# Performance work log

Hardware: AMD Instinct MI355X
Metric: run time of the kernel (lower is better)

Reference implementation:

```python
import jax, jax.numpy as jnp
import numpy as np

N, D, T = 4096, 512, 4096
TEMPERATURE = 0.07
MARGIN = 0.5
CONT_WEIGHT = 1.0
TRIP_WEIGHT = 0.3
EPS = 1e-8        # eps in the log / denominator (matches torch code)
PD_EPS = 1e-6     # F.pairwise_distance default eps added to the difference


def setup_inputs() -> dict:
    key = jax.random.key(0)
    k1, k2, k3 = jax.random.split(key, 3)
    embeddings = jax.random.normal(k1, (N, D), dtype=jnp.float32)
    labels = jax.random.randint(k2, (N,), 0, 256)            # ~16 positives per place
    triplets = jax.random.randint(k3, (T, 3), 0, N)          # (anchor, pos, neg) indices
    return {"embeddings": embeddings, "labels": labels, "triplets": triplets}


def reference(embeddings, labels, triplets):
    # ---- MultiPositiveContrastiveLoss ----
    # F.cosine_similarity normalizes each row with eps=1e-8 on the norm.
    norms = jnp.linalg.norm(embeddings, axis=1, keepdims=True)
    n_emb = embeddings / jnp.maximum(norms, EPS)
    sim = (n_emb @ n_emb.T) / TEMPERATURE                    # [N, N]

    pos_mask = (labels[:, None] == labels[None, :]).astype(embeddings.dtype)
    pos_mask = pos_mask * (1.0 - jnp.eye(sim.shape[0], dtype=embeddings.dtype))

    exp_sim = jnp.exp(sim)
    pos_sum = (exp_sim * pos_mask).sum(axis=1)
    total_sum = exp_sim.sum(axis=1)
    loss = -jnp.log(pos_sum / (total_sum + EPS) + EPS)

    valid = pos_mask.sum(axis=1) > 0
    cnt = valid.sum()
    cont_loss = jnp.where(
        cnt > 0,
        jnp.where(valid, loss, 0.0).sum() / jnp.maximum(cnt, 1).astype(loss.dtype),
        jnp.zeros((), loss.dtype),
    )

    # ---- TripletLoss, vectorized over all triplets (replaces Python loop) ----
    a = embeddings[triplets[:, 0]]   # [T, D]
    p = embeddings[triplets[:, 1]]
    ng = embeddings[triplets[:, 2]]
    pos_dist = jnp.linalg.norm(a - p + PD_EPS, axis=1)
    neg_dist = jnp.linalg.norm(a - ng + PD_EPS, axis=1)
    trip_loss = jnp.maximum(pos_dist - neg_dist + MARGIN, 0.0).mean()

    total = CONT_WEIGHT * cont_loss + TRIP_WEIGHT * trip_loss
    return (total, cont_loss, trip_loss)
```

## Files before the change

kernel.cpp:

```cpp
#include <hip/hip_runtime.h>

#define NN 4096
#define DD 512
#define TT 4096

typedef __bf16 bf16x8 __attribute__((ext_vector_type(8)));
typedef float f32x4 __attribute__((ext_vector_type(4)));

constexpr float INV_TEMP = 1.0f / 0.07f;

__global__ __launch_bounds__(256) void k_normalize(const float* __restrict__ emb,
                                                   __bf16* __restrict__ nemb) {
    int wave = threadIdx.x >> 6, lane = threadIdx.x & 63;
    int row = blockIdx.x * 4 + wave;
    const float4* src = (const float4*)(emb + (size_t)row * DD);
    float4 x0 = src[lane * 2 + 0];
    float4 x1 = src[lane * 2 + 1];
    float ss = x0.x * x0.x + x0.y * x0.y + x0.z * x0.z + x0.w * x0.w +
               x1.x * x1.x + x1.y * x1.y + x1.z * x1.z + x1.w * x1.w;
    #pragma unroll
    for (int m = 1; m < 64; m <<= 1) ss += __shfl_xor(ss, m, 64);
    float inv = 1.0f / fmaxf(sqrtf(ss), 1e-8f);
    bf16x8 v;
    v[0] = (__bf16)(x0.x * inv); v[1] = (__bf16)(x0.y * inv);
    v[2] = (__bf16)(x0.z * inv); v[3] = (__bf16)(x0.w * inv);
    v[4] = (__bf16)(x1.x * inv); v[5] = (__bf16)(x1.y * inv);
    v[6] = (__bf16)(x1.z * inv); v[7] = (__bf16)(x1.w * inv);
    *(bf16x8*)(nemb + (size_t)row * DD + lane * 8) = v;
}

__global__ __launch_bounds__(256) void k_contrast(const __bf16* __restrict__ nemb,
                                                  const int* __restrict__ labels,
                                                  float* __restrict__ posP,
                                                  float* __restrict__ totP,
                                                  float* __restrict__ cntP) {
    __shared__ __attribute__((aligned(16))) __bf16 aSm[128 * 32];
    __shared__ __attribute__((aligned(16))) __bf16 bSm[128 * 32];
    __shared__ int rlab[128];
    __shared__ int clab[128];

    int tid = threadIdx.x;
    int lane = tid & 63, wave = tid >> 6;
    int wr = wave >> 1, wc = wave & 1;
    int l15 = lane & 15, quad = lane >> 4;
    int rowblk = blockIdx.y, colblk = blockIdx.x;
    int row0 = rowblk * 128, col0 = colblk * 128;

    if (tid < 128) rlab[tid] = labels[row0 + tid];
    else           clab[tid - 128] = labels[col0 + tid - 128];

    f32x4 acc[4][4];
    #pragma unroll
    for (int r = 0; r < 4; ++r)
        #pragma unroll
        for (int c = 0; c < 4; ++c) {
            f32x4 z = {0.0f, 0.0f, 0.0f, 0.0f};
            acc[r][c] = z;
        }

    int rA = tid >> 2, sA = tid & 3;

    for (int kt = 0; kt < 16; ++kt) {
        int kb = kt * 32;
        uint4 a0 = *(const uint4*)(nemb + (size_t)(row0 + rA) * DD + kb + sA * 8);
        uint4 a1 = *(const uint4*)(nemb + (size_t)(row0 + rA + 64) * DD + kb + sA * 8);
        uint4 b0 = *(const uint4*)(nemb + (size_t)(col0 + rA) * DD + kb + sA * 8);
        uint4 b1 = *(const uint4*)(nemb + (size_t)(col0 + rA + 64) * DD + kb + sA * 8);
        __syncthreads();
        ((uint4*)aSm)[tid] = a0;
        ((uint4*)aSm)[tid + 256] = a1;
        ((uint4*)bSm)[tid] = b0;
        ((uint4*)bSm)[tid + 256] = b1;
        __syncthreads();

        bf16x8 af[4], bfr[4];
        #pragma unroll
        for (int r = 0; r < 4; ++r)
            af[r] = *(const bf16x8*)(aSm + (wr * 64 + r * 16 + l15) * 32 + quad * 8);
        #pragma unroll
        for (int c = 0; c < 4; ++c)
            bfr[c] = *(const bf16x8*)(bSm + (wc * 64 + c * 16 + l15) * 32 + quad * 8);
        #pragma unroll
        for (int r = 0; r < 4; ++r)
            #pragma unroll
            for (int c = 0; c < 4; ++c)
                acc[r][c] = __builtin_amdgcn_mfma_f32_16x16x32_bf16(af[r], bfr[c], acc[r][c], 0, 0, 0);
    }

    int cl[4];
    #pragma unroll
    for (int c = 0; c < 4; ++c) cl[c] = clab[wc * 64 + c * 16 + l15];

    #pragma unroll
    for (int r = 0; r < 4; ++r) {
        float tv[4] = {0, 0, 0, 0}, pv[4] = {0, 0, 0, 0}, cv[4] = {0, 0, 0, 0};
        int gibase = row0 + wr * 64 + r * 16 + quad * 4;
        int rl[4];
        #pragma unroll
        for (int v = 0; v < 4; ++v) rl[v] = rlab[wr * 64 + r * 16 + quad * 4 + v];
        #pragma unroll
        for (int c = 0; c < 4; ++c) {
            int gj = col0 + wc * 64 + c * 16 + l15;
            #pragma unroll
            for (int v = 0; v < 4; ++v) {
                float e = __expf(acc[r][c][v] * INV_TEMP);
                tv[v] += e;
                bool match = (rl[v] == cl[c]) && ((gibase + v) != gj);
                pv[v] += match ? e : 0.0f;
                cv[v] += match ? 1.0f : 0.0f;
            }
        }
        #pragma unroll
        for (int m = 1; m < 16; m <<= 1) {
            #pragma unroll
            for (int v = 0; v < 4; ++v) {
                tv[v] += __shfl_xor(tv[v], m, 64);
                pv[v] += __shfl_xor(pv[v], m, 64);
                cv[v] += __shfl_xor(cv[v], m, 64);
            }
        }
        if (l15 == 0) {
            #pragma unroll
            for (int v = 0; v < 4; ++v) {
                int gr = gibase + v;
                int idx = gr * 64 + colblk * 2 + wc;
                posP[idx] = pv[v];
                totP[idx] = tv[v];
                cntP[idx] = cv[v];
            }
        }
    }
}

__global__ __launch_bounds__(256) void k_triplet(const float* __restrict__ emb,
                                                 const int* __restrict__ trip,
                                                 float* __restrict__ tl) {
    int wave = threadIdx.x >> 6, lane = threadIdx.x & 63;
    int t = blockIdx.x * 4 + wave;
    int ia = trip[t * 3 + 0], ip = trip[t * 3 + 1], ig = trip[t * 3 + 2];
    const float4* pa = (const float4*)(emb + (size_t)ia * DD);
    const float4* pp = (const float4*)(emb + (size_t)ip * DD);
    const float4* pn = (const float4*)(emb + (size_t)ig * DD);
    float d1 = 0.0f, d2 = 0.0f;
    #pragma unroll
    for (int j = 0; j < 2; ++j) {
        float4 a = pa[lane * 2 + j];
        float4 p = pp[lane * 2 + j];
        float4 n = pn[lane * 2 + j];
        float dx;
        dx = a.x - p.x + 1e-6f; d1 += dx * dx;
        dx = a.y - p.y + 1e-6f; d1 += dx * dx;
        dx = a.z - p.z + 1e-6f; d1 += dx * dx;
        dx = a.w - p.w + 1e-6f; d1 += dx * dx;
        dx = a.x - n.x + 1e-6f; d2 += dx * dx;
        dx = a.y - n.y + 1e-6f; d2 += dx * dx;
        dx = a.z - n.z + 1e-6f; d2 += dx * dx;
        dx = a.w - n.w + 1e-6f; d2 += dx * dx;
    }
    #pragma unroll
    for (int m = 1; m < 64; m <<= 1) {
        d1 += __shfl_xor(d1, m, 64);
        d2 += __shfl_xor(d2, m, 64);
    }
    if (lane == 0) tl[t] = fmaxf(sqrtf(d1) - sqrtf(d2) + 0.5f, 0.0f);
}

__global__ __launch_bounds__(256) void k_rowloss(const float* __restrict__ posP,
                                                 const float* __restrict__ totP,
                                                 const float* __restrict__ cntP,
                                                 float* __restrict__ rloss,
                                                 float* __restrict__ rvalid) {
    int row = blockIdx.x * 256 + threadIdx.x;
    float p = 0.0f, t = 0.0f, c = 0.0f;
    for (int i = 0; i < 64; ++i) {
        p += posP[row * 64 + i];
        t += totP[row * 64 + i];
        c += cntP[row * 64 + i];
    }
    float loss = -logf(p / (t + 1e-8f) + 1e-8f);
    bool valid = c > 0.0f;
    rloss[row] = valid ? loss : 0.0f;
    rvalid[row] = valid ? 1.0f : 0.0f;
}

__global__ __launch_bounds__(256) void k_final(const float* __restrict__ rloss,
                                               const float* __restrict__ rvalid,
                                               const float* __restrict__ tl,
                                               float* __restrict__ out) {
    int tid = threadIdx.x;
    float sl = 0.0f, sv = 0.0f, st = 0.0f;
    for (int i = tid; i < NN; i += 256) {
        sl += rloss[i];
        sv += rvalid[i];
        st += tl[i];
    }
    #pragma unroll
    for (int m = 1; m < 64; m <<= 1) {
        sl += __shfl_xor(sl, m, 64);
        sv += __shfl_xor(sv, m, 64);
        st += __shfl_xor(st, m, 64);
    }
    __shared__ float red[3][4];
    int lane = tid & 63, wave = tid >> 6;
    if (lane == 0) { red[0][wave] = sl; red[1][wave] = sv; red[2][wave] = st; }
    __syncthreads();
    if (tid == 0) {
        float SL = red[0][0] + red[0][1] + red[0][2] + red[0][3];
        float SV = red[1][0] + red[1][1] + red[1][2] + red[1][3];
        float ST = red[2][0] + red[2][1] + red[2][2] + red[2][3];
        float cont = (SV > 0.0f) ? (SL / SV) : 0.0f;
        float trip = ST * (1.0f / (float)TT);
        out[0] = cont + 0.3f * trip;
        out[1] = cont;
        out[2] = trip;
    }
}

extern "C" void kernel_launch(void* const* d_in, const int* in_sizes, int n_in,
                              void* d_out, int out_size, void* d_ws, size_t ws_size,
                              hipStream_t stream) {
    const float* emb = (const float*)d_in[0];
    const int* labels = (const int*)d_in[1];
    const int* trips = (const int*)d_in[2];
    float* out = (float*)d_out;
    char* ws = (char*)d_ws;

    __bf16* nemb  = (__bf16*)(ws);
    float* posP   = (float*)(ws + 4194304);
    float* totP   = (float*)(ws + 5242880);
    float* cntP   = (float*)(ws + 6291456);
    float* rloss  = (float*)(ws + 7340032);
    float* rvalid = (float*)(ws + 7356416);
    float* tl     = (float*)(ws + 7372800);

    k_normalize<<<NN / 4, 256, 0, stream>>>(emb, nemb);
    k_contrast<<<dim3(32, 32), 256, 0, stream>>>(nemb, labels, posP, totP, cntP);
    k_triplet<<<TT / 4, 256, 0, stream>>>(emb, trips, tl);
    k_rowloss<<<NN / 256, 256, 0, stream>>>(posP, totP, cntP, rloss, rvalid);
    k_final<<<1, 256, 0, stream>>>(rloss, rvalid, tl, out);
}
```

Before: 117.4 us.

## Exploit similarity-matrix symmetry by computing only upper-triangular tiles

The contrastive kernel now launches 528 blocks over the upper-triangular 128x128 tiles of the similarity matrix instead of all 1024. Each block decodes its tile coordinates from a triangular index. Off-diagonal tiles also reduce their exp values along columns and write those partial sums into the transposed tile's slots, so about half of the GEMM and exp work is skipped. This costs extra column reductions, extra partial-sum writes, and some integer/sqrt index math per block.

```diff
diff --git a/kernel.cpp b/kernel.cpp
--- a/kernel.cpp
+++ b/kernel.cpp
@@ -43,8 +43,15 @@
     int lane = tid & 63, wave = tid >> 6;
     int wr = wave >> 1, wc = wave & 1;
     int l15 = lane & 15, quad = lane >> 4;
-    int rowblk = blockIdx.y, colblk = blockIdx.x;
+
+    int idx = blockIdx.x;
+    int cb = (int)((sqrtf(8.0f * (float)idx + 1.0f) - 1.0f) * 0.5f);
+    while ((cb + 1) * (cb + 2) / 2 <= idx) ++cb;
+    while (cb * (cb + 1) / 2 > idx) --cb;
+    int rb = idx - cb * (cb + 1) / 2;
+    int rowblk = rb, colblk = cb;
     int row0 = rowblk * 128, col0 = colblk * 128;
+    bool offd = (rowblk != colblk);
 
     if (tid < 128) rlab[tid] = labels[row0 + tid];
     else           clab[tid - 128] = labels[col0 + tid - 128];
@@ -91,6 +98,8 @@
     #pragma unroll
     for (int c = 0; c < 4; ++c) cl[c] = clab[wc * 64 + c * 16 + l15];
 
+    float tT[4] = {0, 0, 0, 0}, pT[4] = {0, 0, 0, 0}, cT[4] = {0, 0, 0, 0};
+
     #pragma unroll
     for (int r = 0; r < 4; ++r) {
         float tv[4] = {0, 0, 0, 0}, pv[4] = {0, 0, 0, 0}, cv[4] = {0, 0, 0, 0};
@@ -104,10 +113,11 @@
             #pragma unroll
             for (int v = 0; v < 4; ++v) {
                 float e = __expf(acc[r][c][v] * INV_TEMP);
-                tv[v] += e;
                 bool match = (rl[v] == cl[c]) && ((gibase + v) != gj);
-                pv[v] += match ? e : 0.0f;
-                cv[v] += match ? 1.0f : 0.0f;
+                float me = match ? e : 0.0f;
+                float mc = match ? 1.0f : 0.0f;
+                tv[v] += e;  pv[v] += me;  cv[v] += mc;
+                tT[c] += e;  pT[c] += me;  cT[c] += mc;
             }
         }
         #pragma unroll
@@ -123,10 +133,32 @@
             #pragma unroll
             for (int v = 0; v < 4; ++v) {
                 int gr = gibase + v;
-                int idx = gr * 64 + colblk * 2 + wc;
-                posP[idx] = pv[v];
-                totP[idx] = tv[v];
-                cntP[idx] = cv[v];
+                int oidx = gr * 64 + colblk * 2 + wc;
+                posP[oidx] = pv[v];
+                totP[oidx] = tv[v];
+                cntP[oidx] = cv[v];
+            }
+        }
+    }
+
+    if (offd) {
+        #pragma unroll
+        for (int m = 16; m < 64; m <<= 1) {
+            #pragma unroll
+            for (int c = 0; c < 4; ++c) {
+                tT[c] += __shfl_xor(tT[c], m, 64);
+                pT[c] += __shfl_xor(pT[c], m, 64);
+                cT[c] += __shfl_xor(cT[c], m, 64);
+            }
+        }
+        if (quad == 0) {
+            #pragma unroll
+            for (int c = 0; c < 4; ++c) {
+                int gj = col0 + wc * 64 + c * 16 + l15;
+                int oidx = gj * 64 + rowblk * 2 + wr;
+                posP[oidx] = pT[c];
+                totP[oidx] = tT[c];
+                cntP[oidx] = cT[c];
             }
         }
     }
@@ -234,7 +266,7 @@
     float* tl     = (float*)(ws + 7372800);
 
     k_normalize<<<NN / 4, 256, 0, stream>>>(emb, nemb);
-    k_contrast<<<dim3(32, 32), 256, 0, stream>>>(nemb, labels, posP, totP, cntP);
+    k_contrast<<<528, 256, 0, stream>>>(nemb, labels, posP, totP, cntP);
     k_triplet<<<TT / 4, 256, 0, stream>>>(emb, trips, tl);
     k_rowloss<<<NN / 256, 256, 0, stream>>>(posP, totP, cntP, rloss, rvalid);
     k_final<<<1, 256, 0, stream>>>(rloss, rvalid, tl, out);
```

Result: slower. 127.8 us (+8.8%).
